# Optimization experiments

Hardware: AMD Instinct MI355X
Metric: run time of the kernel (lower is better)

Reference implementation:

```python
import jax, jax.numpy as jnp
import numpy as np

B, T, E = 4, 2048, 1024
H, D = 16, 64


def setup_inputs() -> dict:
    key = jax.random.key(0)
    ks = jax.random.split(key, 7)
    scale = 1.0 / np.sqrt(E)
    return {
        "query": jax.random.normal(ks[0], (B, T, E), jnp.float32),
        "key_": jax.random.normal(ks[1], (B, T, E), jnp.float32),
        "value": jax.random.normal(ks[2], (B, T, E), jnp.float32),
        # nn.Linear weights have shape (out_features, in_features); y = x @ W.T
        "Wq": jax.random.normal(ks[3], (H * D, E), jnp.float32) * scale,
        "Wk": jax.random.normal(ks[4], (H * D, E), jnp.float32) * scale,
        "Wv": jax.random.normal(ks[5], (H * D, E), jnp.float32) * scale,
        "Wo": jax.random.normal(ks[6], (E, H * D), jnp.float32) * scale,
    }


def reference(query, key_, value, Wq, Wk, Wv, Wo):
    # eval mode: dropout is identity
    Bq, Tq, _ = query.shape
    Q = (query @ Wq.T).reshape(Bq, Tq, H, D).transpose(0, 2, 1, 3)   # [B,H,T,D]
    K = (key_ @ Wk.T).reshape(Bq, -1, H, D).transpose(0, 2, 1, 3)    # [B,H,S,D]
    V = (value @ Wv.T).reshape(Bq, -1, H, D).transpose(0, 2, 1, 3)   # [B,H,S,D]
    scores = jnp.einsum("bhtd,bhsd->bhts", Q, K) / jnp.sqrt(jnp.float32(D))
    attn_prob = jax.nn.softmax(scores, axis=-1)                      # [B,H,T,S]
    attn_vec = jnp.einsum("bhts,bhsd->bhtd", attn_prob, V)           # [B,H,T,D]
    x = attn_vec.transpose(0, 2, 1, 3).reshape(Bq, Tq, H * D) @ Wo.T # [B,T,E]
    # need_weights=True, average_attn_weights=True -> mean over heads
    return x, attn_prob.mean(axis=1)
```

## Files before the change

kernel.cpp:

```cpp
#include <hip/hip_runtime.h>
#include <math.h>

#define HH 16
#define DD 64
#define TS 2048
#define EE 1024
#define BB 4
#define MS 12.0f

typedef __attribute__((ext_vector_type(8))) __bf16 bf16x8;
typedef __attribute__((ext_vector_type(8))) _Float16 f16x8;
typedef __attribute__((ext_vector_type(4))) float f32x4;

#define LBAR() asm volatile("s_waitcnt lgkmcnt(0)\n\ts_barrier" ::: "memory")

__device__ __forceinline__ f32x4 mm3(bf16x8 ah, bf16x8 al, bf16x8 bh, bf16x8 bl, f32x4 c) {
    c = __builtin_amdgcn_mfma_f32_16x16x32_bf16(ah, bh, c, 0, 0, 0);
    c = __builtin_amdgcn_mfma_f32_16x16x32_bf16(ah, bl, c, 0, 0, 0);
    c = __builtin_amdgcn_mfma_f32_16x16x32_bf16(al, bh, c, 0, 0, 0);
    return c;
}

__device__ __forceinline__ void gll16(const void* g, void* l) {
    __builtin_amdgcn_global_load_lds(
        (const __attribute__((address_space(1))) unsigned int*)g,
        (__attribute__((address_space(3))) unsigned int*)l, 16, 0, 0);
}

__device__ __forceinline__ unsigned pk2(float p) {
    __bf16 h = (__bf16)p;
    __bf16 l = (__bf16)(p - (float)h);
    return ((unsigned)__builtin_bit_cast(unsigned short, h) << 16) |
            (unsigned)__builtin_bit_cast(unsigned short, l);
}
__device__ __forceinline__ float upk_hi(unsigned u) { return __builtin_bit_cast(float, u & 0xffff0000u); }
__device__ __forceinline__ float upk_lo(unsigned u) { return __builtin_bit_cast(float, u << 16); }

__device__ __forceinline__ bf16x8 sel_frag(uint4 a, uint4 b, unsigned s) {
    uint4 r;
    r.x = __builtin_amdgcn_perm(a.y, a.x, s);
    r.y = __builtin_amdgcn_perm(a.w, a.z, s);
    r.z = __builtin_amdgcn_perm(b.y, b.x, s);
    r.w = __builtin_amdgcn_perm(b.w, b.z, s);
    return __builtin_bit_cast(bf16x8, r);
}

__device__ __forceinline__ void split8(const float* __restrict__ src,
    __bf16* __restrict__ hi, __bf16* __restrict__ lo, size_t i)
{
    float4 a = *(const float4*)(src + i);
    float4 b = *(const float4*)(src + i + 4);
    float v[8] = {a.x, a.y, a.z, a.w, b.x, b.y, b.z, b.w};
    bf16x8 h, l;
    #pragma unroll
    for (int j = 0; j < 8; ++j) {
        __bf16 x = (__bf16)v[j];
        h[j] = x;
        l[j] = (__bf16)(v[j] - (float)x);
    }
    *(bf16x8*)(hi + i) = h;
    *(bf16x8*)(lo + i) = l;
}

__global__ __launch_bounds__(256) void splitX(
    const float* __restrict__ q, const float* __restrict__ k, const float* __restrict__ v,
    __bf16* __restrict__ qh, __bf16* __restrict__ ql,
    __bf16* __restrict__ kh, __bf16* __restrict__ kl,
    __bf16* __restrict__ vh, __bf16* __restrict__ vl)
{
    const int z = blockIdx.y;
    const float* src = z == 0 ? q : z == 1 ? k : v;
    __bf16* hi = z == 0 ? qh : z == 1 ? kh : vh;
    __bf16* lo = z == 0 ? ql : z == 1 ? kl : vl;
    size_t i = ((size_t)blockIdx.x * 256 + threadIdx.x) * 8;
    split8(src, hi, lo, i);
}

__global__ __launch_bounds__(256) void splitW(
    const float* __restrict__ wq, const float* __restrict__ wk,
    const float* __restrict__ wv, const float* __restrict__ wo,
    __bf16* __restrict__ qh, __bf16* __restrict__ ql,
    __bf16* __restrict__ kh, __bf16* __restrict__ kl,
    __bf16* __restrict__ vh, __bf16* __restrict__ vl,
    __bf16* __restrict__ oh, __bf16* __restrict__ ol)
{
    const int z = blockIdx.y;
    const float* src = z == 0 ? wq : z == 1 ? wk : z == 2 ? wv : wo;
    __bf16* hi = z == 0 ? qh : z == 1 ? kh : z == 2 ? vh : oh;
    __bf16* lo = z == 0 ? ql : z == 1 ? kl : z == 2 ? vl : ol;
    size_t i = ((size_t)blockIdx.x * 256 + threadIdx.x) * 8;
    split8(src, hi, lo, i);
}

template<int OMODE>
__global__ __launch_bounds__(256) void gemm3(
    const __bf16* __restrict__ Ah, const __bf16* __restrict__ Al,
    const __bf16* __restrict__ Bh, const __bf16* __restrict__ Bl,
    float* __restrict__ Cf, __bf16* __restrict__ Ch, __bf16* __restrict__ Cl,
    int M, int N, int K)
{
    __shared__ __bf16 sA[2][128 * 32];
    __shared__ __bf16 sB[2][128 * 32];
    const int tid = threadIdx.x, wave = tid >> 6, lane = tid & 63;
    const int quad = lane >> 4, l15 = lane & 15;
    const int m0 = blockIdx.y * 128, n0 = blockIdx.x * 128;
    const int wm = (wave >> 1) * 64, wn = (wave & 1) * 64;
    const int srow = lane >> 2, scol = (lane & 3) * 8;

    f32x4 acc[4][4];
    #pragma unroll
    for (int i = 0; i < 4; ++i)
        #pragma unroll
        for (int j = 0; j < 4; ++j)
            acc[i][j] = (f32x4){0.f, 0.f, 0.f, 0.f};

    for (int k0 = 0; k0 < K; k0 += 32) {
        __syncthreads();
        #pragma unroll
        for (int i = 0; i < 2; ++i) {
            int c = wave * 2 + i;
            size_t ga = (size_t)(m0 + c * 16 + srow) * K + k0 + scol;
            size_t gb = (size_t)(n0 + c * 16 + srow) * K + k0 + scol;
            gll16(Ah + ga, &sA[0][c * 512]);
            gll16(Al + ga, &sA[1][c * 512]);
            gll16(Bh + gb, &sB[0][c * 512]);
            gll16(Bl + gb, &sB[1][c * 512]);
        }
        __syncthreads();
        bf16x8 fAh[4], fAl[4], fBh[4], fBl[4];
        #pragma unroll
        for (int mb = 0; mb < 4; ++mb) {
            int r = (wm + mb * 16 + l15) * 32 + quad * 8;
            fAh[mb] = *(const bf16x8*)&sA[0][r];
            fAl[mb] = *(const bf16x8*)&sA[1][r];
        }
        #pragma unroll
        for (int nb = 0; nb < 4; ++nb) {
            int r = (wn + nb * 16 + l15) * 32 + quad * 8;
            fBh[nb] = *(const bf16x8*)&sB[0][r];
            fBl[nb] = *(const bf16x8*)&sB[1][r];
        }
        #pragma unroll
        for (int mb = 0; mb < 4; ++mb)
            #pragma unroll
            for (int nb = 0; nb < 4; ++nb)
                acc[mb][nb] = mm3(fAh[mb], fAl[mb], fBh[nb], fBl[nb], acc[mb][nb]);
    }

    #pragma unroll
    for (int mb = 0; mb < 4; ++mb)
        #pragma unroll
        for (int nb = 0; nb < 4; ++nb)
            #pragma unroll
            for (int r = 0; r < 4; ++r) {
                int m = m0 + wm + mb * 16 + quad * 4 + r;
                int n = n0 + wn + nb * 16 + l15;
                float v = acc[mb][nb][r];
                Cf[(size_t)m * N + n] = v;
            }
}

__global__ __launch_bounds__(256) void gemmQKV(
    const __bf16* __restrict__ xqh, const __bf16* __restrict__ xql,
    const __bf16* __restrict__ xkh, const __bf16* __restrict__ xkl,
    const __bf16* __restrict__ xvh, const __bf16* __restrict__ xvl,
    const __bf16* __restrict__ wqh, const __bf16* __restrict__ wql,
    const __bf16* __restrict__ wkh, const __bf16* __restrict__ wkl,
    const __bf16* __restrict__ wvh, const __bf16* __restrict__ wvl,
    __bf16* __restrict__ Qh, __bf16* __restrict__ Ql,
    __bf16* __restrict__ Kh, __bf16* __restrict__ Kl,
    __bf16* __restrict__ Vh, __bf16* __restrict__ Vl)
{
    const int z = blockIdx.z;
    const __bf16* Ah = z == 0 ? xqh : z == 1 ? xkh : xvh;
    const __bf16* Al = z == 0 ? xql : z == 1 ? xkl : xvl;
    const __bf16* Bh = z == 0 ? wqh : z == 1 ? wkh : wvh;
    const __bf16* Bl = z == 0 ? wql : z == 1 ? wkl : wvl;
    __bf16* Ch = z == 0 ? Qh : z == 1 ? Kh : Vh;
    __bf16* Cl = z == 0 ? Ql : z == 1 ? Kl : Vl;
    const int K = EE;

    __shared__ __bf16 sA[2][128 * 32];
    __shared__ __bf16 sB[2][128 * 32];
    const int tid = threadIdx.x, wave = tid >> 6, lane = tid & 63;
    const int quad = lane >> 4, l15 = lane & 15;
    const int m0 = blockIdx.y * 128, n0 = blockIdx.x * 128;
    const int wm = (wave >> 1) * 64, wn = (wave & 1) * 64;
    const int srow = lane >> 2, scol = (lane & 3) * 8;

    f32x4 acc[4][4];
    #pragma unroll
    for (int i = 0; i < 4; ++i)
        #pragma unroll
        for (int j = 0; j < 4; ++j)
            acc[i][j] = (f32x4){0.f, 0.f, 0.f, 0.f};

    for (int k0 = 0; k0 < K; k0 += 32) {
        __syncthreads();
        #pragma unroll
        for (int i = 0; i < 2; ++i) {
            int c = wave * 2 + i;
            size_t ga = (size_t)(m0 + c * 16 + srow) * K + k0 + scol;
            size_t gb = (size_t)(n0 + c * 16 + srow) * K + k0 + scol;
            gll16(Ah + ga, &sA[0][c * 512]);
            gll16(Al + ga, &sA[1][c * 512]);
            gll16(Bh + gb, &sB[0][c * 512]);
            gll16(Bl + gb, &sB[1][c * 512]);
        }
        __syncthreads();
        bf16x8 fAh[4], fAl[4], fBh[4], fBl[4];
        #pragma unroll
        for (int mb = 0; mb < 4; ++mb) {
            int r = (wm + mb * 16 + l15) * 32 + quad * 8;
            fAh[mb] = *(const bf16x8*)&sA[0][r];
            fAl[mb] = *(const bf16x8*)&sA[1][r];
        }
        #pragma unroll
        for (int nb = 0; nb < 4; ++nb) {
            int r = (wn + nb * 16 + l15) * 32 + quad * 8;
            fBh[nb] = *(const bf16x8*)&sB[0][r];
            fBl[nb] = *(const bf16x8*)&sB[1][r];
        }
        #pragma unroll
        for (int mb = 0; mb < 4; ++mb)
            #pragma unroll
            for (int nb = 0; nb < 4; ++nb)
                acc[mb][nb] = mm3(fAh[mb], fAl[mb], fBh[nb], fBl[nb], acc[mb][nb]);
    }

    #pragma unroll
    for (int mb = 0; mb < 4; ++mb)
        #pragma unroll
        for (int nb = 0; nb < 4; ++nb)
            #pragma unroll
            for (int r = 0; r < 4; ++r) {
                int m = m0 + wm + mb * 16 + quad * 4 + r;
                int n = n0 + wn + nb * 16 + l15;
                float v = acc[mb][nb][r];
                int b = m >> 11, t = m & (TS - 1);
                int h = n >> 6,  d = n & (DD - 1);
                __bf16 hi = (__bf16)v;
                __bf16 lo = (__bf16)(v - (float)hi);
                size_t hbase = ((size_t)b * HH + h) * TS * DD;
                size_t off;
                if (z == 2)
                    off = hbase + (size_t)(((d >> 4) * 64 + (t >> 5)) * 512
                          + (((t >> 3) & 3) * 16 + (d & 15)) * 8 + (d & 7) * 0 + (t & 7));
                else
                    off = hbase + (size_t)(((t >> 4) * 2 + (d >> 5)) * 512
                          + (((d >> 3) & 3) * 16 + (t & 15)) * 8 + (d & 7));
                Ch[off] = hi;
                Cl[off] = lo;
            }
}

__global__ __launch_bounds__(256) void attnF(
    const __bf16* __restrict__ Qh, const __bf16* __restrict__ Ql,
    const __bf16* __restrict__ Kh, const __bf16* __restrict__ Kl,
    const __bf16* __restrict__ VhT, const __bf16* __restrict__ VlT,
    __bf16* __restrict__ avh, __bf16* __restrict__ avl,
    float* __restrict__ out1, _Float16* __restrict__ pp)
{
    __shared__ unsigned Pt[4][32][68];
    const int tid = threadIdx.x, wave = tid >> 6, lane = tid & 63;
    const int quad = lane >> 4, l15 = lane & 15;
    const int linear = blockIdx.x + 64 * blockIdx.y + 256 * blockIdx.z;
    const int bg = (linear & 7) + 8 * (linear >> 9);
    const int tt = (linear >> 3) & 63;
    const int b = bg & 3, g = bg >> 2;
    const int t0 = tt * 32;
    const int h = g * 4 + wave;
    const size_t hoff = (size_t)(b * HH + h);
    const __bf16* qhp = Qh + hoff * TS * DD;
    const __bf16* qlp = Ql + hoff * TS * DD;
    const __bf16* khp = Kh + hoff * TS * DD;
    const __bf16* klp = Kl + hoff * TS * DD;
    const __bf16* vhp = VhT + hoff * DD * TS;
    const __bf16* vlp = VlT + hoff * DD * TS;
    _Float16* myp = pp + (size_t)(g - 1) * ((size_t)BB * TS * TS);

    const int loff = (quad * 16 + l15) * 8;

    bf16x8 fqh[2][2], fql[2][2];
    #pragma unroll
    for (int tb = 0; tb < 2; ++tb)
        #pragma unroll
        for (int ks = 0; ks < 2; ++ks) {
            size_t o = (size_t)((((t0 >> 4) + tb) * 2 + ks) * 512 + loff);
            fqh[tb][ks] = *(const bf16x8*)(qhp + o);
            fql[tb][ks] = *(const bf16x8*)(qlp + o);
        }

    float lacc[2][4];
    #pragma unroll
    for (int tb = 0; tb < 2; ++tb)
        #pragma unroll
        for (int r = 0; r < 4; ++r) lacc[tb][r] = 0.f;

    for (int st = 0; st < 32; ++st) {
        bf16x8 kh[4][2], kl[4][2];
        #pragma unroll
        for (int sb = 0; sb < 4; ++sb) {
            const int kt = ((st * 4 + sb) * 2) * 512 + loff;
            kh[sb][0] = *(const bf16x8*)(khp + kt);
            kh[sb][1] = *(const bf16x8*)(khp + kt + 512);
            kl[sb][0] = *(const bf16x8*)(klp + kt);
            kl[sb][1] = *(const bf16x8*)(klp + kt + 512);
        }
        #pragma unroll
        for (int sb = 0; sb < 4; ++sb)
            #pragma unroll
            for (int tb = 0; tb < 2; ++tb) {
                f32x4 c = (f32x4){0.f, 0.f, 0.f, 0.f};
                c = mm3(fqh[tb][0], fql[tb][0], kh[sb][0], kl[sb][0], c);
                c = mm3(fqh[tb][1], fql[tb][1], kh[sb][1], kl[sb][1], c);
                #pragma unroll
                for (int r = 0; r < 4; ++r)
                    lacc[tb][r] += __expf(c[r] * 0.125f - MS);
            }
    }
    float rf[2][4];
    #pragma unroll
    for (int tb = 0; tb < 2; ++tb)
        #pragma unroll
        for (int r = 0; r < 4; ++r) {
            float v = lacc[tb][r];
            v += __shfl_xor(v, 1);
            v += __shfl_xor(v, 2);
            v += __shfl_xor(v, 4);
            v += __shfl_xor(v, 8);
            rf[tb][r] = 1.0f / v;
        }

    f32x4 oacc[2][4];
    #pragma unroll
    for (int tb = 0; tb < 2; ++tb)
        #pragma unroll
        for (int db = 0; db < 4; ++db) oacc[tb][db] = (f32x4){0.f, 0.f, 0.f, 0.f};

    for (int st = 0; st < 32; ++st) {
        bf16x8 kh[4][2], kl[4][2];
        #pragma unroll
        for (int sb = 0; sb < 4; ++sb) {
            const int kt = ((st * 4 + sb) * 2) * 512 + loff;
            kh[sb][0] = *(const bf16x8*)(khp + kt);
            kh[sb][1] = *(const bf16x8*)(khp + kt + 512);
            kl[sb][0] = *(const bf16x8*)(klp + kt);
            kl[sb][1] = *(const bf16x8*)(klp + kt + 512);
        }
        #pragma unroll
        for (int sb = 0; sb < 4; ++sb)
            #pragma unroll
            for (int tb = 0; tb < 2; ++tb) {
                f32x4 c = (f32x4){0.f, 0.f, 0.f, 0.f};
                c = mm3(fqh[tb][0], fql[tb][0], kh[sb][0], kl[sb][0], c);
                c = mm3(fqh[tb][1], fql[tb][1], kh[sb][1], kl[sb][1], c);
                #pragma unroll
                for (int r = 0; r < 4; ++r) {
                    float p = __expf(c[r] * 0.125f - MS) * rf[tb][r];
                    Pt[wave][tb * 16 + quad * 4 + r][sb * 16 + l15] = pk2(p);
                }
            }
        LBAR();

        bf16x8 vh[4][2], vl[4][2];
        #pragma unroll
        for (int db = 0; db < 4; ++db) {
            const int vt = (db * 64 + st * 2) * 512 + loff;
            vh[db][0] = *(const bf16x8*)(vhp + vt);
            vh[db][1] = *(const bf16x8*)(vhp + vt + 512);
            vl[db][0] = *(const bf16x8*)(vlp + vt);
            vl[db][1] = *(const bf16x8*)(vlp + vt + 512);
        }

        bf16x8 fph[2][2], fpl[2][2];
        #pragma unroll
        for (int tb = 0; tb < 2; ++tb)
            #pragma unroll
            for (int ks = 0; ks < 2; ++ks) {
                const unsigned* ppt = &Pt[wave][tb * 16 + l15][ks * 32 + quad * 8];
                uint4 a = *(const uint4*)ppt;
                uint4 bq = *(const uint4*)(ppt + 4);
                fph[tb][ks] = sel_frag(a, bq, 0x07060302u);
                fpl[tb][ks] = sel_frag(a, bq, 0x05040100u);
            }

        {
            int row = tid >> 3, s8 = (tid & 7) * 8;
            float vs[8] = {0.f, 0.f, 0.f, 0.f, 0.f, 0.f, 0.f, 0.f};
            #pragma unroll
            for (int w = 0; w < 4; ++w) {
                const unsigned* pw = &Pt[w][row][s8];
                uint4 a = *(const uint4*)pw;
                uint4 bq = *(const uint4*)(pw + 4);
                unsigned uu[8] = {a.x, a.y, a.z, a.w, bq.x, bq.y, bq.z, bq.w};
                #pragma unroll
                for (int j = 0; j < 8; ++j)
                    vs[j] += upk_hi(uu[j]) + upk_lo(uu[j]);
            }
            size_t off = ((size_t)b * TS + t0 + row) * TS + st * 64 + s8;
            if (g == 0) {
                float4 o0, o1v;
                o0.x = vs[0] * 0.0625f; o0.y = vs[1] * 0.0625f;
                o0.z = vs[2] * 0.0625f; o0.w = vs[3] * 0.0625f;
                o1v.x = vs[4] * 0.0625f; o1v.y = vs[5] * 0.0625f;
                o1v.z = vs[6] * 0.0625f; o1v.w = vs[7] * 0.0625f;
                *(float4*)(out1 + off) = o0;
                *(float4*)(out1 + off + 4) = o1v;
            } else {
                f16x8 hv;
                #pragma unroll
                for (int j = 0; j < 8; ++j)
                    hv[j] = (_Float16)(vs[j] * 0.0625f);
                *(f16x8*)(myp + off) = hv;
            }
        }

        #pragma unroll
        for (int db = 0; db < 4; ++db)
            #pragma unroll
            for (int tb = 0; tb < 2; ++tb) {
                f32x4 o = oacc[tb][db];
                o = mm3(fph[tb][0], fpl[tb][0], vh[db][0], vl[db][0], o);
                o = mm3(fph[tb][1], fpl[tb][1], vh[db][1], vl[db][1], o);
                oacc[tb][db] = o;
            }
        LBAR();
    }

    #pragma unroll
    for (int tb = 0; tb < 2; ++tb)
        #pragma unroll
        for (int db = 0; db < 4; ++db)
            #pragma unroll
            for (int r = 0; r < 4; ++r) {
                int row = t0 + tb * 16 + quad * 4 + r;
                int col = h * 64 + db * 16 + l15;
                float v = oacc[tb][db][r];
                __bf16 hi = (__bf16)v;
                size_t o = ((size_t)b * TS + row) * EE + col;
                avh[o] = hi;
                avl[o] = (__bf16)(v - (float)hi);
            }
}

__global__ __launch_bounds__(256) void redk(float* __restrict__ out1,
    const _Float16* __restrict__ pp)
{
    const size_t P = (size_t)BB * TS * TS;
    size_t i = ((size_t)blockIdx.x * 256 + threadIdx.x) * 8;
    float4 a = *(const float4*)(out1 + i);
    float4 c = *(const float4*)(out1 + i + 4);
    f16x8 q1 = *(const f16x8*)(pp + i);
    f16x8 q2 = *(const f16x8*)(pp + P + i);
    f16x8 q3 = *(const f16x8*)(pp + 2 * P + i);
    a.x += (float)q1[0] + (float)q2[0] + (float)q3[0];
    a.y += (float)q1[1] + (float)q2[1] + (float)q3[1];
    a.z += (float)q1[2] + (float)q2[2] + (float)q3[2];
    a.w += (float)q1[3] + (float)q2[3] + (float)q3[3];
    c.x += (float)q1[4] + (float)q2[4] + (float)q3[4];
    c.y += (float)q1[5] + (float)q2[5] + (float)q3[5];
    c.z += (float)q1[6] + (float)q2[6] + (float)q3[6];
    c.w += (float)q1[7] + (float)q2[7] + (float)q3[7];
    *(float4*)(out1 + i) = a;
    *(float4*)(out1 + i + 4) = c;
}

extern "C" void kernel_launch(void* const* d_in, const int* in_sizes, int n_in,
                              void* d_out, int out_size, void* d_ws, size_t ws_size,
                              hipStream_t stream)
{
    const float* query = (const float*)d_in[0];
    const float* key_  = (const float*)d_in[1];
    const float* value = (const float*)d_in[2];
    const float* Wq    = (const float*)d_in[3];
    const float* Wk    = (const float*)d_in[4];
    const float* Wv    = (const float*)d_in[5];
    const float* Wo    = (const float*)d_in[6];

    float* out0 = (float*)d_out;
    float* out1 = out0 + (size_t)BB * TS * EE;

    char* base = (char*)d_ws;
    const size_t U = 16777216;
    __bf16* xqh = (__bf16*)(base + 0 * U);
    __bf16* xql = (__bf16*)(base + 1 * U);
    __bf16* xkh = (__bf16*)(base + 2 * U);
    __bf16* xkl = (__bf16*)(base + 3 * U);
    __bf16* xvh = (__bf16*)(base + 4 * U);
    __bf16* xvl = (__bf16*)(base + 5 * U);
    __bf16* Qhp = (__bf16*)(base + 6 * U);
    __bf16* Qlp = (__bf16*)(base + 7 * U);
    __bf16* Khp = (__bf16*)(base + 8 * U);
    __bf16* Klp = (__bf16*)(base + 9 * U);
    __bf16* VhT = (__bf16*)(base + 10 * U);
    __bf16* VlT = (__bf16*)(base + 11 * U);
    __bf16* avh = (__bf16*)(base + 12 * U);
    __bf16* avl = (__bf16*)(base + 13 * U);
    __bf16* wqh = (__bf16*)(base + 14 * U);
    __bf16* wql = wqh + 1048576;
    __bf16* wkh = wql + 1048576;
    __bf16* wkl = wkh + 1048576;
    __bf16* wvh = wkl + 1048576;
    __bf16* wvl = wvh + 1048576;
    __bf16* woh = wvl + 1048576;
    __bf16* wol = woh + 1048576;
    _Float16* pp = (_Float16*)(base + 0 * U);

    splitX<<<dim3(4096, 3), 256, 0, stream>>>(query, key_, value,
                                              xqh, xql, xkh, xkl, xvh, xvl);
    splitW<<<dim3(512, 4), 256, 0, stream>>>(Wq, Wk, Wv, Wo,
                                             wqh, wql, wkh, wkl, wvh, wvl, woh, wol);

    gemmQKV<<<dim3(8, 64, 3), 256, 0, stream>>>(xqh, xql, xkh, xkl, xvh, xvl,
                                                wqh, wql, wkh, wkl, wvh, wvl,
                                                Qhp, Qlp, Khp, Klp, VhT, VlT);

    attnF<<<dim3(64, 4, 4), 256, 0, stream>>>(Qhp, Qlp, Khp, Klp, VhT, VlT,
                                              avh, avl, out1, pp);

    redk<<<8192, 256, 0, stream>>>(out1, pp);

    gemm3<0><<<dim3(8, 64), 256, 0, stream>>>(avh, avl, woh, wol, out0,
                                              nullptr, nullptr, 8192, 1024, 1024);
}
```

Baseline: 857.5 us.

## Merge split kernels, fuse head-mean reduction into output GEMM, cheapen exp and packing

Folds the two input/weight split kernels into a single launch. It also merges the partial head-average reduction into the output projection GEMM grid as extra blocks, so the two run concurrently, and removes two launches. In the attention kernel, the exp is rewritten as a single fma plus native exp2, the hi/lo bf16 packing uses bit masking (the high half is now truncated rather than rounded), and the hi+lo unpack-sum uses a bf16 dot2 instruction when it is available. These trade a small amount of numerical behaviour for fewer instructions and fewer launches.

```diff
diff --git a/kernel.cpp b/kernel.cpp
--- a/kernel.cpp
+++ b/kernel.cpp
@@ -9,8 +9,25 @@
 #define MS 12.0f
 
 typedef __attribute__((ext_vector_type(8))) __bf16 bf16x8;
+typedef __attribute__((ext_vector_type(2))) __bf16 bf16x2;
 typedef __attribute__((ext_vector_type(8))) _Float16 f16x8;
 typedef __attribute__((ext_vector_type(4))) float f32x4;
+
+#if defined(__has_builtin)
+#if __has_builtin(__builtin_amdgcn_fdot2_f32_bf16)
+#define HAS_DOT2 1
+#endif
+#if __has_builtin(__builtin_amdgcn_exp2f)
+#define EXP2(x) __builtin_amdgcn_exp2f(x)
+#endif
+#endif
+#ifndef EXP2
+#define EXP2(x) exp2f(x)
+#endif
+
+__device__ __forceinline__ float pexp(float c) {
+    return EXP2(__builtin_fmaf(c, 0.18033688011112042f, -17.312340490667562f));
+}
 
 #define LBAR() asm volatile("s_waitcnt lgkmcnt(0)\n\ts_barrier" ::: "memory")
 
@@ -28,10 +45,11 @@
 }
 
 __device__ __forceinline__ unsigned pk2(float p) {
-    __bf16 h = (__bf16)p;
-    __bf16 l = (__bf16)(p - (float)h);
-    return ((unsigned)__builtin_bit_cast(unsigned short, h) << 16) |
-            (unsigned)__builtin_bit_cast(unsigned short, l);
+    unsigned pu = __builtin_bit_cast(unsigned, p);
+    unsigned hb = pu & 0xffff0000u;
+    float l = p - __builtin_bit_cast(float, hb);
+    __bf16 lb = (__bf16)l;
+    return hb | (unsigned)__builtin_bit_cast(unsigned short, lb);
 }
 __device__ __forceinline__ float upk_hi(unsigned u) { return __builtin_bit_cast(float, u & 0xffff0000u); }
 __device__ __forceinline__ float upk_lo(unsigned u) { return __builtin_bit_cast(float, u << 16); }
@@ -62,102 +80,36 @@
     *(bf16x8*)(lo + i) = l;
 }
 
-__global__ __launch_bounds__(256) void splitX(
+__global__ __launch_bounds__(256) void splitAll(
     const float* __restrict__ q, const float* __restrict__ k, const float* __restrict__ v,
-    __bf16* __restrict__ qh, __bf16* __restrict__ ql,
-    __bf16* __restrict__ kh, __bf16* __restrict__ kl,
-    __bf16* __restrict__ vh, __bf16* __restrict__ vl)
-{
-    const int z = blockIdx.y;
-    const float* src = z == 0 ? q : z == 1 ? k : v;
-    __bf16* hi = z == 0 ? qh : z == 1 ? kh : vh;
-    __bf16* lo = z == 0 ? ql : z == 1 ? kl : vl;
-    size_t i = ((size_t)blockIdx.x * 256 + threadIdx.x) * 8;
-    split8(src, hi, lo, i);
-}
-
-__global__ __launch_bounds__(256) void splitW(
     const float* __restrict__ wq, const float* __restrict__ wk,
     const float* __restrict__ wv, const float* __restrict__ wo,
-    __bf16* __restrict__ qh, __bf16* __restrict__ ql,
-    __bf16* __restrict__ kh, __bf16* __restrict__ kl,
-    __bf16* __restrict__ vh, __bf16* __restrict__ vl,
-    __bf16* __restrict__ oh, __bf16* __restrict__ ol)
+    __bf16* __restrict__ xqh, __bf16* __restrict__ xql,
+    __bf16* __restrict__ xkh, __bf16* __restrict__ xkl,
+    __bf16* __restrict__ xvh, __bf16* __restrict__ xvl,
+    __bf16* __restrict__ wqh, __bf16* __restrict__ wql,
+    __bf16* __restrict__ wkh, __bf16* __restrict__ wkl,
+    __bf16* __restrict__ wvh, __bf16* __restrict__ wvl,
+    __bf16* __restrict__ woh, __bf16* __restrict__ wol)
 {
-    const int z = blockIdx.y;
-    const float* src = z == 0 ? wq : z == 1 ? wk : z == 2 ? wv : wo;
-    __bf16* hi = z == 0 ? qh : z == 1 ? kh : z == 2 ? vh : oh;
-    __bf16* lo = z == 0 ? ql : z == 1 ? kl : z == 2 ? vl : ol;
-    size_t i = ((size_t)blockIdx.x * 256 + threadIdx.x) * 8;
-    split8(src, hi, lo, i);
-}
-
-template<int OMODE>
-__global__ __launch_bounds__(256) void gemm3(
-    const __bf16* __restrict__ Ah, const __bf16* __restrict__ Al,
-    const __bf16* __restrict__ Bh, const __bf16* __restrict__ Bl,
-    float* __restrict__ Cf, __bf16* __restrict__ Ch, __bf16* __restrict__ Cl,
-    int M, int N, int K)
-{
-    __shared__ __bf16 sA[2][128 * 32];
-    __shared__ __bf16 sB[2][128 * 32];
-    const int tid = threadIdx.x, wave = tid >> 6, lane = tid & 63;
-    const int quad = lane >> 4, l15 = lane & 15;
-    const int m0 = blockIdx.y * 128, n0 = blockIdx.x * 128;
-    const int wm = (wave >> 1) * 64, wn = (wave & 1) * 64;
-    const int srow = lane >> 2, scol = (lane & 3) * 8;
-
-    f32x4 acc[4][4];
-    #pragma unroll
-    for (int i = 0; i < 4; ++i)
-        #pragma unroll
-        for (int j = 0; j < 4; ++j)
-            acc[i][j] = (f32x4){0.f, 0.f, 0.f, 0.f};
-
-    for (int k0 = 0; k0 < K; k0 += 32) {
-        __syncthreads();
-        #pragma unroll
-        for (int i = 0; i < 2; ++i) {
-            int c = wave * 2 + i;
-            size_t ga = (size_t)(m0 + c * 16 + srow) * K + k0 + scol;
-            size_t gb = (size_t)(n0 + c * 16 + srow) * K + k0 + scol;
-            gll16(Ah + ga, &sA[0][c * 512]);
-            gll16(Al + ga, &sA[1][c * 512]);
-            gll16(Bh + gb, &sB[0][c * 512]);
-            gll16(Bl + gb, &sB[1][c * 512]);
-        }
-        __syncthreads();
-        bf16x8 fAh[4], fAl[4], fBh[4], fBl[4];
-        #pragma unroll
-        for (int mb = 0; mb < 4; ++mb) {
-            int r = (wm + mb * 16 + l15) * 32 + quad * 8;
-            fAh[mb] = *(const bf16x8*)&sA[0][r];
-            fAl[mb] = *(const bf16x8*)&sA[1][r];
-        }
-        #pragma unroll
-        for (int nb = 0; nb < 4; ++nb) {
-            int r = (wn + nb * 16 + l15) * 32 + quad * 8;
-            fBh[nb] = *(const bf16x8*)&sB[0][r];
-            fBl[nb] = *(const bf16x8*)&sB[1][r];
-        }
-        #pragma unroll
-        for (int mb = 0; mb < 4; ++mb)
-            #pragma unroll
-            for (int nb = 0; nb < 4; ++nb)
-                acc[mb][nb] = mm3(fAh[mb], fAl[mb], fBh[nb], fBl[nb], acc[mb][nb]);
-    }
-
-    #pragma unroll
-    for (int mb = 0; mb < 4; ++mb)
-        #pragma unroll
-        for (int nb = 0; nb < 4; ++nb)
-            #pragma unroll
-            for (int r = 0; r < 4; ++r) {
-                int m = m0 + wm + mb * 16 + quad * 4 + r;
-                int n = n0 + wn + nb * 16 + l15;
-                float v = acc[mb][nb][r];
-                Cf[(size_t)m * N + n] = v;
-            }
+    const int id = blockIdx.x;
+    const float* src;
+    __bf16 *hi, *lo;
+    size_t base;
+    if (id < 12288) {
+        int z = id >> 12, loc = id & 4095;
+        src = z == 0 ? q : z == 1 ? k : v;
+        hi  = z == 0 ? xqh : z == 1 ? xkh : xvh;
+        lo  = z == 0 ? xql : z == 1 ? xkl : xvl;
+        base = (size_t)loc * 2048;
+    } else {
+        int w = (id - 12288) >> 9, loc = (id - 12288) & 511;
+        src = w == 0 ? wq : w == 1 ? wk : w == 2 ? wv : wo;
+        hi  = w == 0 ? wqh : w == 1 ? wkh : w == 2 ? wvh : woh;
+        lo  = w == 0 ? wql : w == 1 ? wkl : w == 2 ? wvl : wol;
+        base = (size_t)loc * 2048;
+    }
+    split8(src, hi, lo, base + threadIdx.x * 8);
 }
 
 __global__ __launch_bounds__(256) void gemmQKV(
@@ -245,7 +197,7 @@
                 size_t off;
                 if (z == 2)
                     off = hbase + (size_t)(((d >> 4) * 64 + (t >> 5)) * 512
-                          + (((t >> 3) & 3) * 16 + (d & 15)) * 8 + (d & 7) * 0 + (t & 7));
+                          + (((t >> 3) & 3) * 16 + (d & 15)) * 8 + (t & 7));
                 else
                     off = hbase + (size_t)(((t >> 4) * 2 + (d >> 5)) * 512
                           + (((d >> 3) & 3) * 16 + (t & 15)) * 8 + (d & 7));
@@ -316,7 +268,7 @@
                 c = mm3(fqh[tb][1], fql[tb][1], kh[sb][1], kl[sb][1], c);
                 #pragma unroll
                 for (int r = 0; r < 4; ++r)
-                    lacc[tb][r] += __expf(c[r] * 0.125f - MS);
+                    lacc[tb][r] += pexp(c[r]);
             }
     }
     float rf[2][4];
@@ -357,7 +309,7 @@
                 c = mm3(fqh[tb][1], fql[tb][1], kh[sb][1], kl[sb][1], c);
                 #pragma unroll
                 for (int r = 0; r < 4; ++r) {
-                    float p = __expf(c[r] * 0.125f - MS) * rf[tb][r];
+                    float p = pexp(c[r]) * rf[tb][r];
                     Pt[wave][tb * 16 + quad * 4 + r][sb * 16 + l15] = pk2(p);
                 }
             }
@@ -388,6 +340,9 @@
         {
             int row = tid >> 3, s8 = (tid & 7) * 8;
             float vs[8] = {0.f, 0.f, 0.f, 0.f, 0.f, 0.f, 0.f, 0.f};
+#ifdef HAS_DOT2
+            const bf16x2 one2 = {(__bf16)1.0f, (__bf16)1.0f};
+#endif
             #pragma unroll
             for (int w = 0; w < 4; ++w) {
                 const unsigned* pw = &Pt[w][row][s8];
@@ -395,8 +350,14 @@
                 uint4 bq = *(const uint4*)(pw + 4);
                 unsigned uu[8] = {a.x, a.y, a.z, a.w, bq.x, bq.y, bq.z, bq.w};
                 #pragma unroll
-                for (int j = 0; j < 8; ++j)
+                for (int j = 0; j < 8; ++j) {
+#ifdef HAS_DOT2
+                    vs[j] = __builtin_amdgcn_fdot2_f32_bf16(
+                        __builtin_bit_cast(bf16x2, uu[j]), one2, vs[j], false);
+#else
                     vs[j] += upk_hi(uu[j]) + upk_lo(uu[j]);
+#endif
+                }
             }
             size_t off = ((size_t)b * TS + t0 + row) * TS + st * 64 + s8;
             if (g == 0) {
@@ -444,26 +405,94 @@
             }
 }
 
-__global__ __launch_bounds__(256) void redk(float* __restrict__ out1,
-    const _Float16* __restrict__ pp)
+__global__ __launch_bounds__(256) void gemmO(
+    const __bf16* __restrict__ Ah, const __bf16* __restrict__ Al,
+    const __bf16* __restrict__ Bh, const __bf16* __restrict__ Bl,
+    float* __restrict__ Cf, float* __restrict__ out1,
+    const _Float16* __restrict__ pp, int M, int N, int K)
 {
-    const size_t P = (size_t)BB * TS * TS;
-    size_t i = ((size_t)blockIdx.x * 256 + threadIdx.x) * 8;
-    float4 a = *(const float4*)(out1 + i);
-    float4 c = *(const float4*)(out1 + i + 4);
-    f16x8 q1 = *(const f16x8*)(pp + i);
-    f16x8 q2 = *(const f16x8*)(pp + P + i);
-    f16x8 q3 = *(const f16x8*)(pp + 2 * P + i);
-    a.x += (float)q1[0] + (float)q2[0] + (float)q3[0];
-    a.y += (float)q1[1] + (float)q2[1] + (float)q3[1];
-    a.z += (float)q1[2] + (float)q2[2] + (float)q3[2];
-    a.w += (float)q1[3] + (float)q2[3] + (float)q3[3];
-    c.x += (float)q1[4] + (float)q2[4] + (float)q3[4];
-    c.y += (float)q1[5] + (float)q2[5] + (float)q3[5];
-    c.z += (float)q1[6] + (float)q2[6] + (float)q3[6];
-    c.w += (float)q1[7] + (float)q2[7] + (float)q3[7];
-    *(float4*)(out1 + i) = a;
-    *(float4*)(out1 + i + 4) = c;
+    __shared__ __bf16 sA[2][128 * 32];
+    __shared__ __bf16 sB[2][128 * 32];
+    const int tid = threadIdx.x;
+
+    if (blockIdx.x >= 8) {
+        const size_t P = (size_t)BB * TS * TS;
+        size_t r = (size_t)(blockIdx.x - 8) + 128 * blockIdx.y;
+        size_t i = (r * 256 + tid) * 8;
+        float4 a = *(const float4*)(out1 + i);
+        float4 c = *(const float4*)(out1 + i + 4);
+        f16x8 q1 = *(const f16x8*)(pp + i);
+        f16x8 q2 = *(const f16x8*)(pp + P + i);
+        f16x8 q3 = *(const f16x8*)(pp + 2 * P + i);
+        a.x += (float)q1[0] + (float)q2[0] + (float)q3[0];
+        a.y += (float)q1[1] + (float)q2[1] + (float)q3[1];
+        a.z += (float)q1[2] + (float)q2[2] + (float)q3[2];
+        a.w += (float)q1[3] + (float)q2[3] + (float)q3[3];
+        c.x += (float)q1[4] + (float)q2[4] + (float)q3[4];
+        c.y += (float)q1[5] + (float)q2[5] + (float)q3[5];
+        c.z += (float)q1[6] + (float)q2[6] + (float)q3[6];
+        c.w += (float)q1[7] + (float)q2[7] + (float)q3[7];
+        *(float4*)(out1 + i) = a;
+        *(float4*)(out1 + i + 4) = c;
+        return;
+    }
+
+    const int wave = tid >> 6, lane = tid & 63;
+    const int quad = lane >> 4, l15 = lane & 15;
+    const int m0 = blockIdx.y * 128, n0 = blockIdx.x * 128;
+    const int wm = (wave >> 1) * 64, wn = (wave & 1) * 64;
+    const int srow = lane >> 2, scol = (lane & 3) * 8;
+
+    f32x4 acc[4][4];
+    #pragma unroll
+    for (int i = 0; i < 4; ++i)
+        #pragma unroll
+        for (int j = 0; j < 4; ++j)
+            acc[i][j] = (f32x4){0.f, 0.f, 0.f, 0.f};
+
+    for (int k0 = 0; k0 < K; k0 += 32) {
+        __syncthreads();
+        #pragma unroll
+        for (int i = 0; i < 2; ++i) {
+            int c = wave * 2 + i;
+            size_t ga = (size_t)(m0 + c * 16 + srow) * K + k0 + scol;
+            size_t gb = (size_t)(n0 + c * 16 + srow) * K + k0 + scol;
+            gll16(Ah + ga, &sA[0][c * 512]);
+            gll16(Al + ga, &sA[1][c * 512]);
+            gll16(Bh + gb, &sB[0][c * 512]);
+            gll16(Bl + gb, &sB[1][c * 512]);
+        }
+        __syncthreads();
+        bf16x8 fAh[4], fAl[4], fBh[4], fBl[4];
+        #pragma unroll
+        for (int mb = 0; mb < 4; ++mb) {
+            int r = (wm + mb * 16 + l15) * 32 + quad * 8;
+            fAh[mb] = *(const bf16x8*)&sA[0][r];
+            fAl[mb] = *(const bf16x8*)&sA[1][r];
+        }
+        #pragma unroll
+        for (int nb = 0; nb < 4; ++nb) {
+            int r = (wn + nb * 16 + l15) * 32 + quad * 8;
+            fBh[nb] = *(const bf16x8*)&sB[0][r];
+            fBl[nb] = *(const bf16x8*)&sB[1][r];
+        }
+        #pragma unroll
+        for (int mb = 0; mb < 4; ++mb)
+            #pragma unroll
+            for (int nb = 0; nb < 4; ++nb)
+                acc[mb][nb] = mm3(fAh[mb], fAl[mb], fBh[nb], fBl[nb], acc[mb][nb]);
+    }
+
+    #pragma unroll
+    for (int mb = 0; mb < 4; ++mb)
+        #pragma unroll
+        for (int nb = 0; nb < 4; ++nb)
+            #pragma unroll
+            for (int r = 0; r < 4; ++r) {
+                int m = m0 + wm + mb * 16 + quad * 4 + r;
+                int n = n0 + wn + nb * 16 + l15;
+                Cf[(size_t)m * N + n] = acc[mb][nb][r];
+            }
 }
 
 extern "C" void kernel_launch(void* const* d_in, const int* in_sizes, int n_in,
@@ -507,10 +536,9 @@
     __bf16* wol = woh + 1048576;
     _Float16* pp = (_Float16*)(base + 0 * U);
 
-    splitX<<<dim3(4096, 3), 256, 0, stream>>>(query, key_, value,
-                                              xqh, xql, xkh, xkl, xvh, xvl);
-    splitW<<<dim3(512, 4), 256, 0, stream>>>(Wq, Wk, Wv, Wo,
-                                             wqh, wql, wkh, wkl, wvh, wvl, woh, wol);
+    splitAll<<<14336, 256, 0, stream>>>(query, key_, value, Wq, Wk, Wv, Wo,
+                                        xqh, xql, xkh, xkl, xvh, xvl,
+                                        wqh, wql, wkh, wkl, wvh, wvl, woh, wol);
 
     gemmQKV<<<dim3(8, 64, 3), 256, 0, stream>>>(xqh, xql, xkh, xkl, xvh, xvl,
                                                 wqh, wql, wkh, wkl, wvh, wvl,
@@ -519,8 +547,6 @@
     attnF<<<dim3(64, 4, 4), 256, 0, stream>>>(Qhp, Qlp, Khp, Klp, VhT, VlT,
                                               avh, avl, out1, pp);
 
-    redk<<<8192, 256, 0, stream>>>(out1, pp);
-
-    gemm3<0><<<dim3(8, 64), 256, 0, stream>>>(avh, avl, woh, wol, out0,
-                                              nullptr, nullptr, 8192, 1024, 1024);
-}
+    gemmO<<<dim3(136, 64), 256, 0, stream>>>(avh, avl, woh, wol, out0, out1, pp,
+                                             8192, 1024, 1024);
+}
```

After: 849.5 us. No clear change (-0.9%).
